# Kernel tuning notes

Measured on AMD Instinct MI355X. Metric: run time of the kernel, lower is better.

The kernel has to match this reference:

```python
import jax, jax.numpy as jnp
import numpy as np

B, C, H, W = 16, 256, 32, 32
NUM_HEADS = 8
GN_GROUPS = 8
GN_EPS = 1e-5


def setup_inputs() -> dict:
    key = jax.random.key(0)
    k1, k2, k3 = jax.random.split(key, 3)
    x = jax.random.normal(k1, (B, C, H, W), dtype=jnp.float32)
    # 1x1 convs == channel matmuls; store weights as [out_ch, in_ch]
    w_qkv = jax.random.normal(k2, (3 * C, C), dtype=jnp.float32) * (C ** -0.5)
    w_proj = jax.random.normal(k3, (C, C), dtype=jnp.float32) * (C ** -0.5)
    gn_gamma = jnp.ones((C,), dtype=jnp.float32)
    gn_beta = jnp.zeros((C,), dtype=jnp.float32)
    return {"x": x, "w_qkv": w_qkv, "w_proj": w_proj, "gn_gamma": gn_gamma, "gn_beta": gn_beta}


def reference(x, w_qkv, w_proj, gn_gamma, gn_beta):
    b, c, h, w = x.shape
    nh = NUM_HEADS
    hd = c // nh
    hw = h * w
    residual = x

    # qkv 1x1 conv (no bias): [b,3c,h,w]
    qkv = jnp.einsum('oc,bchw->bohw', w_qkv, x)
    # reshape(b,3,nh,hd,hw) then permute(1,0,2,4,3) -> (3,b,nh,hw,hd)
    qkv = qkv.reshape(b, 3, nh, hd, hw).transpose(1, 0, 2, 4, 3)
    q, k, v = qkv[0], qkv[1], qkv[2]  # each [b,nh,hw,hd]

    scale = hd ** -0.5
    attn = jnp.einsum('bnid,bnjd->bnij', q, k) * scale  # [b,nh,hw,hw]
    attn = attn - jnp.max(attn, axis=-1, keepdims=True)
    attn = jax.nn.softmax(attn, axis=-1)
    out = jnp.einsum('bnij,bnjd->bnid', attn, v)  # [b,nh,hw,hd]

    # permute(0,1,3,2) -> [b,nh,hd,hw] -> [b,c,h,w]
    out = out.transpose(0, 1, 3, 2).reshape(b, c, h, w)

    # proj 1x1 conv
    out = jnp.einsum('oc,bchw->bohw', w_proj, out)

    # GroupNorm(8, c)
    g = GN_GROUPS
    og = out.reshape(b, g, c // g, h, w)
    mean = jnp.mean(og, axis=(2, 3, 4), keepdims=True)
    var = jnp.var(og, axis=(2, 3, 4), keepdims=True)
    og = (og - mean) * jax.lax.rsqrt(var + GN_EPS)
    out = og.reshape(b, c, h, w) * gn_gamma[None, :, None, None] + gn_beta[None, :, None, None]

    return out + residual
```

## Files before the change

### kernel.cpp

```cpp
#include <hip/hip_runtime.h>
#include <hip/hip_bf16.h>
#include <math.h>

#define BATCH 16
#define CCH 256
#define HW 1024
#define NH 8
#define HD 32
#define QSCALE 0.25500526954123462f

typedef __attribute__((ext_vector_type(8))) short bf16x8;
typedef __attribute__((ext_vector_type(4))) short bf16x4;
typedef __attribute__((ext_vector_type(4))) float f32x4;
typedef __attribute__((ext_vector_type(2))) unsigned int u32x2;

__device__ __forceinline__ unsigned short bf16bits(float f) {
  __hip_bfloat16 h = __float2bfloat16(f);
  return *(unsigned short*)&h;
}

__device__ __forceinline__ void gload16(const void* g, void* l) {
  __builtin_amdgcn_global_load_lds(
      (const __attribute__((address_space(1))) unsigned int*)g,
      (__attribute__((address_space(3))) unsigned int*)l, 16, 0, 0);
}

__device__ __forceinline__ unsigned int pack_bf16_trunc(float a, float b) {
  return __builtin_amdgcn_perm(__float_as_uint(b), __float_as_uint(a), 0x07060302u);
}

__global__ __launch_bounds__(256) void cvt_x(const float* __restrict__ x,
                                             unsigned short* __restrict__ xt,
                                             const float* __restrict__ wqkv,
                                             const float* __restrict__ wproj,
                                             unsigned short* __restrict__ wqb,
                                             unsigned short* __restrict__ wpb,
                                             float* __restrict__ gstats) {
  __shared__ unsigned short tile[64][72];
  const int t = threadIdx.x;
  if (blockIdx.y == 4) {
    int wblk = blockIdx.z * 16 + blockIdx.x;
    const float* src;
    unsigned short* dst;
    int i;
    if (wblk < 192) {
      src = wqkv; dst = wqb; i = wblk * 256 + t;
    } else {
      src = wproj; dst = wpb; i = (wblk - 192) * 256 + t;
    }
    float4 v = ((const float4*)src)[i];
    ushort4 o;
    o.x = bf16bits(v.x); o.y = bf16bits(v.y); o.z = bf16bits(v.z); o.w = bf16bits(v.w);
    ((ushort4*)dst)[i] = o;
    if (wblk == 255) gstats[t] = 0.f;
    return;
  }
  const int p0 = blockIdx.x * 64;
  const int c0 = blockIdx.y * 64;
  const int b = blockIdx.z;
  const float* xb = x + (size_t)b * CCH * HW;
#pragma unroll
  for (int i = 0; i < 4; ++i) {
    int f = i * 256 + t;
    int c = f >> 4, p4 = f & 15;
    float4 v = *(const float4*)(xb + (size_t)(c0 + c) * HW + p0 + p4 * 4);
    tile[p4 * 4 + 0][c] = bf16bits(v.x);
    tile[p4 * 4 + 1][c] = bf16bits(v.y);
    tile[p4 * 4 + 2][c] = bf16bits(v.z);
    tile[p4 * 4 + 3][c] = bf16bits(v.w);
  }
  __syncthreads();
  unsigned short* xtb = xt + (size_t)b * HW * CCH;
#pragma unroll
  for (int i = 0; i < 4; ++i) {
    int f = i * 256 + t;
    int p = f >> 4, c4 = f & 15;
    ushort4 v = *(const ushort4*)&tile[p][c4 * 4];
    *(ushort4*)(xtb + (size_t)(p0 + p) * CCH + c0 + c4 * 4) = v;
  }
}

__global__ __launch_bounds__(256) void qkv_mfma(const unsigned short* __restrict__ Wb,
                                                const unsigned short* __restrict__ Xt,
                                                unsigned short* __restrict__ Qb,
                                                unsigned short* __restrict__ Kf,
                                                unsigned short* __restrict__ Vf) {
  __shared__ unsigned short A_l[8 * 128 * 8];
  __shared__ unsigned short B_l[8 * 128 * 8];
  const int t = threadIdx.x;
  const int wave = t >> 6, lane = t & 63;
  const int quad = lane >> 4, n16 = lane & 15;
  const int o0 = blockIdx.x * 128;
  const int p0 = blockIdx.y * 128;
  const int b = blockIdx.z;
  const int wm = (wave >> 1) * 64, wn = (wave & 1) * 64;
  const unsigned short* Xb = Xt + (size_t)b * (HW * CCH);

  f32x4 acc[4][4] = {};
  for (int k0 = 0; k0 < CCH; k0 += 64) {
#pragma unroll
    for (int i = 0; i < 4; ++i) {
      int f = i * 256 + t;
      int kc = f >> 7, m = f & 127;
      int dst = (i * 256 + wave * 64) * 8;
      gload16(Wb + (size_t)(o0 + m) * CCH + k0 + kc * 8, &A_l[dst]);
      gload16(Xb + (size_t)(p0 + m) * CCH + k0 + kc * 8, &B_l[dst]);
    }
    __syncthreads();
#pragma unroll
    for (int ks = 0; ks < 2; ++ks) {
      bf16x8 af[4], bfr[4];
#pragma unroll
      for (int mi = 0; mi < 4; ++mi)
        af[mi] = *(const bf16x8*)&A_l[((ks * 4 + quad) * 128 + wm + mi * 16 + n16) * 8];
#pragma unroll
      for (int ni = 0; ni < 4; ++ni)
        bfr[ni] = *(const bf16x8*)&B_l[((ks * 4 + quad) * 128 + wn + ni * 16 + n16) * 8];
#pragma unroll
      for (int mi = 0; mi < 4; ++mi)
#pragma unroll
        for (int ni = 0; ni < 4; ++ni)
          acc[mi][ni] = __builtin_amdgcn_mfma_f32_16x16x32_bf16(af[mi], bfr[ni], acc[mi][ni], 0, 0, 0);
    }
    __syncthreads();
  }
  const int three = o0 >> 8;
#pragma unroll
  for (int mi = 0; mi < 4; ++mi) {
    int o = o0 + wm + mi * 16 + quad * 4;
    int head = (o >> 5) & 7;
    int d0 = (mi & 1) * 16 + quad * 4;
    size_t bh64 = (size_t)(b * NH + head) * 64;
    size_t bh_base = (size_t)(b * NH + head) * (HW * HD);
#pragma unroll
    for (int ni = 0; ni < 4; ++ni) {
      int p = p0 + wn + ni * 16 + n16;
      if (three == 0) {
        ushort4 st;
        st.x = bf16bits(acc[mi][ni][0] * QSCALE);
        st.y = bf16bits(acc[mi][ni][1] * QSCALE);
        st.z = bf16bits(acc[mi][ni][2] * QSCALE);
        st.w = bf16bits(acc[mi][ni][3] * QSCALE);
        *(ushort4*)&Qb[bh_base + (size_t)p * HD + d0] = st;
      } else if (three == 1) {
        int kb = p >> 4;
        size_t chunk = (bh64 + kb) * 64 + (d0 >> 3) * 16 + n16;
        ushort4 st;
        st.x = bf16bits(acc[mi][ni][0]);
        st.y = bf16bits(acc[mi][ni][1]);
        st.z = bf16bits(acc[mi][ni][2]);
        st.w = bf16bits(acc[mi][ni][3]);
        *(ushort4*)&Kf[chunk * 8 + (d0 & 7)] = st;
      } else {
        int kb = p >> 4;
        size_t base = (bh64 + kb) * 64 + (n16 >> 2) * 16 + quad * 4;
#pragma unroll
        for (int r = 0; r < 4; ++r)
          Vf[(base + r) * 8 + (mi & 1) * 4 + (n16 & 3)] = bf16bits(acc[mi][ni][r]);
      }
    }
  }
}

__global__ __launch_bounds__(256, 4) void attn_mfma(const unsigned short* __restrict__ Q,
                                                    const unsigned short* __restrict__ Kf,
                                                    const unsigned short* __restrict__ Vf,
                                                    unsigned short* __restrict__ Ab) {
  __shared__ unsigned short Ksh[4 * 64 * 8];
  __shared__ unsigned short Vsh[4 * 64 * 8];
  const int t = threadIdx.x;
  const int lane = t & 63;
  const int quad = lane >> 4, n16 = lane & 15;
  const int wave = t >> 6;
  const int id = blockIdx.y * 8 + blockIdx.x;
  const int xcd = id & 7, jj = id >> 3;
  const int bh = xcd * 16 + (jj >> 3);
  const int qtile = jj & 7;
  const int i0w = qtile * 128 + wave * 32;
  const size_t hb = (size_t)bh * (HW * HD);
  const size_t fb = (size_t)bh * 64 * 64 * 8;

  bf16x8 qf0 = *(const bf16x8*)((const short*)Q + hb + (size_t)(i0w + n16) * HD + quad * 8);
  bf16x8 qf1 = *(const bf16x8*)((const short*)Q + hb + (size_t)(i0w + 16 + n16) * HD + quad * 8);
  f32x4 O000 = {0,0,0,0}, O001 = {0,0,0,0}, O010 = {0,0,0,0}, O011 = {0,0,0,0};
  f32x4 O100 = {0,0,0,0}, O101 = {0,0,0,0}, O110 = {0,0,0,0}, O111 = {0,0,0,0};
  const f32x4 zero = {0.f, 0.f, 0.f, 0.f};
  float l0 = 0.f, l1 = 0.f;

  for (int jt = 0; jt < 16; ++jt) {
    gload16(Kf + fb + ((size_t)jt * 4 * 64 + t) * 8, &Ksh[t * 8]);
    gload16(Vf + fb + ((size_t)jt * 4 * 64 + t) * 8, &Vsh[t * 8]);
    __syncthreads();
#pragma unroll
    for (int kk = 0; kk < 4; ++kk) {
      bf16x8 kfr = *(const bf16x8*)&Ksh[(kk * 64 + lane) * 8];
      f32x4 S0 = __builtin_amdgcn_mfma_f32_16x16x32_bf16(kfr, qf0, zero, 0, 0, 0);
      f32x4 S1 = __builtin_amdgcn_mfma_f32_16x16x32_bf16(kfr, qf1, zero, 0, 0, 0);
      float a0 = __builtin_amdgcn_exp2f(S0[0]);
      float a1 = __builtin_amdgcn_exp2f(S0[1]);
      float a2 = __builtin_amdgcn_exp2f(S0[2]);
      float a3 = __builtin_amdgcn_exp2f(S0[3]);
      l0 += (a0 + a1) + (a2 + a3);
      u32x2 pkw0;
      pkw0.x = pack_bf16_trunc(a0, a1);
      pkw0.y = pack_bf16_trunc(a2, a3);
      bf16x4 pf0 = __builtin_bit_cast(bf16x4, pkw0);
      float b0 = __builtin_amdgcn_exp2f(S1[0]);
      float b1 = __builtin_amdgcn_exp2f(S1[1]);
      float b2 = __builtin_amdgcn_exp2f(S1[2]);
      float b3 = __builtin_amdgcn_exp2f(S1[3]);
      l1 += (b0 + b1) + (b2 + b3);
      u32x2 pkw1;
      pkw1.x = pack_bf16_trunc(b0, b1);
      pkw1.y = pack_bf16_trunc(b2, b3);
      bf16x4 pf1 = __builtin_bit_cast(bf16x4, pkw1);
      bf16x8 vv = *(const bf16x8*)&Vsh[(kk * 64 + lane) * 8];
      bf16x4 v0 = __builtin_shufflevector(vv, vv, 0, 1, 2, 3);
      bf16x4 v1 = __builtin_shufflevector(vv, vv, 4, 5, 6, 7);
      if (kk & 1) {
        O001 = __builtin_amdgcn_mfma_f32_16x16x16bf16_1k(pf0, v0, O001, 0, 0, 0);
        O011 = __builtin_amdgcn_mfma_f32_16x16x16bf16_1k(pf0, v1, O011, 0, 0, 0);
        O101 = __builtin_amdgcn_mfma_f32_16x16x16bf16_1k(pf1, v0, O101, 0, 0, 0);
        O111 = __builtin_amdgcn_mfma_f32_16x16x16bf16_1k(pf1, v1, O111, 0, 0, 0);
      } else {
        O000 = __builtin_amdgcn_mfma_f32_16x16x16bf16_1k(pf0, v0, O000, 0, 0, 0);
        O010 = __builtin_amdgcn_mfma_f32_16x16x16bf16_1k(pf0, v1, O010, 0, 0, 0);
        O100 = __builtin_amdgcn_mfma_f32_16x16x16bf16_1k(pf1, v0, O100, 0, 0, 0);
        O110 = __builtin_amdgcn_mfma_f32_16x16x16bf16_1k(pf1, v1, O110, 0, 0, 0);
      }
    }
    __syncthreads();
  }
  f32x4 A0, A1, B0, B1;
#pragma unroll
  for (int r = 0; r < 4; ++r) {
    A0[r] = O000[r] + O001[r]; A1[r] = O010[r] + O011[r];
    B0[r] = O100[r] + O101[r]; B1[r] = O110[r] + O111[r];
  }
  l0 += __shfl_xor(l0, 16, 64); l0 += __shfl_xor(l0, 32, 64);
  l1 += __shfl_xor(l1, 16, 64); l1 += __shfl_xor(l1, 32, 64);
  float linv0 = 1.f / l0, linv1 = 1.f / l1;
  float lq0[4], lq1[4];
#pragma unroll
  for (int r = 0; r < 4; ++r) {
    lq0[r] = __shfl(linv0, quad * 4 + r, 64);
    lq1[r] = __shfl(linv1, quad * 4 + r, 64);
  }
  const int bb = bh >> 3, head = bh & 7;
  unsigned short* dst = Ab + (size_t)bb * (HW * CCH) + head * 32;
#pragma unroll
  for (int r = 0; r < 4; ++r) {
    int p0r = i0w + quad * 4 + r;
    dst[(size_t)p0r * CCH + n16] = bf16bits(A0[r] * lq0[r]);
    dst[(size_t)p0r * CCH + 16 + n16] = bf16bits(A1[r] * lq0[r]);
    int p1r = i0w + 16 + quad * 4 + r;
    dst[(size_t)p1r * CCH + n16] = bf16bits(B0[r] * lq1[r]);
    dst[(size_t)p1r * CCH + 16 + n16] = bf16bits(B1[r] * lq1[r]);
  }
}

__global__ __launch_bounds__(256) void proj_mfma(const unsigned short* __restrict__ Wb,
                                                 const unsigned short* __restrict__ At,
                                                 unsigned short* __restrict__ Pb,
                                                 float* __restrict__ gstats) {
  __shared__ unsigned short A_l[8 * 64 * 8];
  __shared__ unsigned short B_l[8 * 128 * 8];
  const int t = threadIdx.x;
  const int wave = t >> 6, lane = t & 63;
  const int quad = lane >> 4, n16 = lane & 15;
  const int o0 = blockIdx.x * 64;
  const int p0 = blockIdx.y * 128;
  const int b = blockIdx.z;
  const int wm = (wave >> 1) * 32, wn = (wave & 1) * 64;
  const unsigned short* Ax = At + (size_t)b * (HW * CCH);

  f32x4 acc[2][4] = {};
  for (int k0 = 0; k0 < CCH; k0 += 64) {
#pragma unroll
    for (int i = 0; i < 2; ++i) {
      int f = i * 256 + t;
      int kc = f >> 6, m = f & 63;
      int dst = (i * 256 + wave * 64) * 8;
      gload16(Wb + (size_t)(o0 + m) * CCH + k0 + kc * 8, &A_l[dst]);
    }
#pragma unroll
    for (int i = 0; i < 4; ++i) {
      int f = i * 256 + t;
      int kc = f >> 7, m = f & 127;
      int dst = (i * 256 + wave * 64) * 8;
      gload16(Ax + (size_t)(p0 + m) * CCH + k0 + kc * 8, &B_l[dst]);
    }
    __syncthreads();
#pragma unroll
    for (int ks = 0; ks < 2; ++ks) {
      bf16x8 af[2], bfr[4];
#pragma unroll
      for (int mi = 0; mi < 2; ++mi)
        af[mi] = *(const bf16x8*)&A_l[((ks * 4 + quad) * 64 + wm + mi * 16 + n16) * 8];
#pragma unroll
      for (int ni = 0; ni < 4; ++ni)
        bfr[ni] = *(const bf16x8*)&B_l[((ks * 4 + quad) * 128 + wn + ni * 16 + n16) * 8];
#pragma unroll
      for (int mi = 0; mi < 2; ++mi)
#pragma unroll
        for (int ni = 0; ni < 4; ++ni)
          acc[mi][ni] = __builtin_amdgcn_mfma_f32_16x16x32_bf16(af[mi], bfr[ni], acc[mi][ni], 0, 0, 0);
    }
    __syncthreads();
  }
#pragma unroll
  for (int mi = 0; mi < 2; ++mi) {
    int obase = o0 + wm + mi * 16;
    int o = obase + quad * 4;
    float s1 = 0.f, s2 = 0.f;
#pragma unroll
    for (int ni = 0; ni < 4; ++ni) {
      int p = p0 + wn + ni * 16 + n16;
#pragma unroll
      for (int r = 0; r < 4; ++r) {
        float v = acc[mi][ni][r];
        s1 += v; s2 += v * v;
        Pb[(size_t)b * (CCH * HW) + (size_t)(o + r) * HW + p] = bf16bits(v);
      }
    }
#pragma unroll
    for (int m = 1; m < 64; m <<= 1) {
      s1 += __shfl_xor(s1, m, 64);
      s2 += __shfl_xor(s2, m, 64);
    }
    if (lane == 0) {
      int bg = b * 8 + (obase >> 5);
      atomicAdd(&gstats[bg * 2], s1);
      atomicAdd(&gstats[bg * 2 + 1], s2);
    }
  }
}

__global__ __launch_bounds__(256) void gn_apply(const unsigned short* __restrict__ Pb,
                                                const float* __restrict__ x,
                                                const float* __restrict__ gamma,
                                                const float* __restrict__ beta,
                                                const float* __restrict__ gstats,
                                                float* __restrict__ out) {
  int i4 = blockIdx.x * 256 + threadIdx.x;
  int c = (i4 >> 8) & 255;
  int bg = i4 >> 13;
  float mean = gstats[bg * 2] * (1.f / 32768.f);
  float var = gstats[bg * 2 + 1] * (1.f / 32768.f) - mean * mean;
  float inv = rsqrtf(var + 1e-5f);
  float ga = gamma[c] * inv;
  float be = beta[c] - mean * ga;
  ushort4 pu = ((const ushort4*)Pb)[i4];
  float4 xr = ((const float4*)x)[i4];
  float4 o;
  o.x = __uint_as_float((unsigned)pu.x << 16) * ga + be + xr.x;
  o.y = __uint_as_float((unsigned)pu.y << 16) * ga + be + xr.y;
  o.z = __uint_as_float((unsigned)pu.z << 16) * ga + be + xr.z;
  o.w = __uint_as_float((unsigned)pu.w << 16) * ga + be + xr.w;
  ((float4*)out)[i4] = o;
}

extern "C" void kernel_launch(void* const* d_in, const int* in_sizes, int n_in,
                              void* d_out, int out_size, void* d_ws, size_t ws_size,
                              hipStream_t stream) {
  const float* x      = (const float*)d_in[0];
  const float* w_qkv  = (const float*)d_in[1];
  const float* w_proj = (const float*)d_in[2];
  const float* gamma  = (const float*)d_in[3];
  const float* beta   = (const float*)d_in[4];
  float* out = (float*)d_out;

  const size_t SZ = (size_t)BATCH * CCH * HW;
  unsigned short* Pb = (unsigned short*)d_ws;
  unsigned short* Qb  = Pb + SZ;
  unsigned short* Kfr = Qb + SZ;
  unsigned short* Vfr = Kfr + SZ;
  unsigned short* Ab  = Vfr + SZ;
  unsigned short* Xtb = Ab + SZ;
  unsigned short* Wqb = Xtb + SZ;
  unsigned short* Wpb = Wqb + (3 * CCH * CCH);
  float* gstats = (float*)(Wpb + CCH * CCH);

  cvt_x<<<dim3(16, 5, BATCH), 256, 0, stream>>>(x, Xtb, w_qkv, w_proj, Wqb, Wpb, gstats);
  qkv_mfma<<<dim3(6, 8, BATCH), 256, 0, stream>>>(Wqb, Xtb, Qb, Kfr, Vfr);
  attn_mfma<<<dim3(8, 128), 256, 0, stream>>>(Qb, Kfr, Vfr, Ab);
  proj_mfma<<<dim3(4, 8, BATCH), 256, 0, stream>>>(Wpb, Ab, Pb, gstats);
  gn_apply<<<4096, 256, 0, stream>>>(Pb, x, gamma, beta, gstats, out);
}
```

Baseline: 155.9 us.

## Split attention into single-wave blocks loading K/V directly from global

Measured after the change: 160.9 us. 3.2% more time.

```diff
diff --git a/kernel.cpp b/kernel.cpp
--- a/kernel.cpp
+++ b/kernel.cpp
@@ -162,21 +162,17 @@
   }
 }
 
-__global__ __launch_bounds__(256, 4) void attn_mfma(const unsigned short* __restrict__ Q,
-                                                    const unsigned short* __restrict__ Kf,
-                                                    const unsigned short* __restrict__ Vf,
-                                                    unsigned short* __restrict__ Ab) {
-  __shared__ unsigned short Ksh[4 * 64 * 8];
-  __shared__ unsigned short Vsh[4 * 64 * 8];
-  const int t = threadIdx.x;
-  const int lane = t & 63;
+__global__ __launch_bounds__(64, 4) void attn_mfma(const unsigned short* __restrict__ Q,
+                                                   const unsigned short* __restrict__ Kf,
+                                                   const unsigned short* __restrict__ Vf,
+                                                   unsigned short* __restrict__ Ab) {
+  const int lane = threadIdx.x;
   const int quad = lane >> 4, n16 = lane & 15;
-  const int wave = t >> 6;
-  const int id = blockIdx.y * 8 + blockIdx.x;
-  const int xcd = id & 7, jj = id >> 3;
-  const int bh = xcd * 16 + (jj >> 3);
-  const int qtile = jj & 7;
-  const int i0w = qtile * 128 + wave * 32;
+  const int id = blockIdx.x;
+  const int xcd = id & 7, loc = id >> 3;
+  const int bh = xcd * 16 + (loc >> 5);
+  const int q32 = loc & 31;
+  const int i0w = q32 * 32;
   const size_t hb = (size_t)bh * (HW * HD);
   const size_t fb = (size_t)bh * 64 * 64 * 8;
 
@@ -187,13 +183,16 @@
   const f32x4 zero = {0.f, 0.f, 0.f, 0.f};
   float l0 = 0.f, l1 = 0.f;
 
+  const bf16x8* Kp = (const bf16x8*)(Kf + fb);
+  const bf16x8* Vp = (const bf16x8*)(Vf + fb);
+
+#pragma unroll 2
   for (int jt = 0; jt < 16; ++jt) {
-    gload16(Kf + fb + ((size_t)jt * 4 * 64 + t) * 8, &Ksh[t * 8]);
-    gload16(Vf + fb + ((size_t)jt * 4 * 64 + t) * 8, &Vsh[t * 8]);
-    __syncthreads();
 #pragma unroll
     for (int kk = 0; kk < 4; ++kk) {
-      bf16x8 kfr = *(const bf16x8*)&Ksh[(kk * 64 + lane) * 8];
+      const int ci = (jt * 4 + kk) * 64 + lane;
+      bf16x8 kfr = Kp[ci];
+      bf16x8 vv = Vp[ci];
       f32x4 S0 = __builtin_amdgcn_mfma_f32_16x16x32_bf16(kfr, qf0, zero, 0, 0, 0);
       f32x4 S1 = __builtin_amdgcn_mfma_f32_16x16x32_bf16(kfr, qf1, zero, 0, 0, 0);
       float a0 = __builtin_amdgcn_exp2f(S0[0]);
@@ -214,7 +213,6 @@
       pkw1.x = pack_bf16_trunc(b0, b1);
       pkw1.y = pack_bf16_trunc(b2, b3);
       bf16x4 pf1 = __builtin_bit_cast(bf16x4, pkw1);
-      bf16x8 vv = *(const bf16x8*)&Vsh[(kk * 64 + lane) * 8];
       bf16x4 v0 = __builtin_shufflevector(vv, vv, 0, 1, 2, 3);
       bf16x4 v1 = __builtin_shufflevector(vv, vv, 4, 5, 6, 7);
       if (kk & 1) {
@@ -229,7 +227,6 @@
         O110 = __builtin_amdgcn_mfma_f32_16x16x16bf16_1k(pf1, v1, O110, 0, 0, 0);
       }
     }
-    __syncthreads();
   }
   f32x4 A0, A1, B0, B1;
 #pragma unroll
@@ -383,7 +380,7 @@
 
   cvt_x<<<dim3(16, 5, BATCH), 256, 0, stream>>>(x, Xtb, w_qkv, w_proj, Wqb, Wpb, gstats);
   qkv_mfma<<<dim3(6, 8, BATCH), 256, 0, stream>>>(Wqb, Xtb, Qb, Kfr, Vfr);
-  attn_mfma<<<dim3(8, 128), 256, 0, stream>>>(Qb, Kfr, Vfr, Ab);
+  attn_mfma<<<4096, 64, 0, stream>>>(Qb, Kfr, Vfr, Ab);
   proj_mfma<<<dim3(4, 8, BATCH), 256, 0, stream>>>(Wpb, Ab, Pb, gstats);
   gn_apply<<<4096, 256, 0, stream>>>(Pb, x, gamma, beta, gstats, out);
 }
```
